# Kernel optimization log

Measured on AMD Instinct MI355X. Metric: run time of the kernel, lower is better.

## Reference

```python
import jax, jax.numpy as jnp
import numpy as np

N_NODES = 50000
N_EDGES = 800000
IN_CH, HID_CH, OUT_CH = 128, 128, 64


def gcn_conv(x, edge_index, edge_weight, W, b, n_nodes):
    """PyG GCNConv: h = D^-1/2 (A + I) D^-1/2 (x @ W) + b, with weighted edges."""
    src, dst = edge_index[0], edge_index[1]
    loop = jnp.arange(n_nodes)
    src_l = jnp.concatenate([src, loop])               # [E+N]
    dst_l = jnp.concatenate([dst, loop])               # [E+N]
    w_l = jnp.concatenate([edge_weight, jnp.ones((n_nodes,), x.dtype)])
    deg = jax.ops.segment_sum(w_l, dst_l, num_segments=n_nodes)  # weighted in-degree incl. self-loop
    dinv = jnp.where(deg > 0, jax.lax.rsqrt(deg), 0.0)
    norm = dinv[src_l] * w_l * dinv[dst_l]             # [E+N]
    h = x @ W                                          # [N, out]
    msg = h[src_l] * norm[:, None]                     # [E+N, out] gather + scale
    out = jax.ops.segment_sum(msg, dst_l, num_segments=n_nodes)  # scatter-add
    return out + b


def setup_inputs() -> dict:
    key = jax.random.key(0)
    k = jax.random.split(key, 8)
    x = jax.random.normal(k[0], (N_NODES, IN_CH), dtype=jnp.float32)
    edge_index = jax.random.randint(k[1], (2, N_EDGES), 0, N_NODES, dtype=jnp.int64)
    edge_weight = jax.random.uniform(k[2], (N_EDGES,), dtype=jnp.float32)
    s1 = 1.0 / np.sqrt(IN_CH)
    s2 = 1.0 / np.sqrt(HID_CH)
    W1 = jax.random.uniform(k[3], (IN_CH, HID_CH), jnp.float32, -s1, s1)
    b1 = jnp.zeros((HID_CH,), jnp.float32)
    W2 = jax.random.uniform(k[4], (HID_CH, OUT_CH), jnp.float32, -s2, s2)
    b2 = jnp.zeros((OUT_CH,), jnp.float32)
    return {"x": x, "edge_index": edge_index, "edge_weight": edge_weight,
            "W1": W1, "b1": b1, "W2": W2, "b2": b2}


def reference(x, edge_index, edge_weight, W1, b1, W2, b2):
    n = x.shape[0]
    h = jax.nn.relu(gcn_conv(x, edge_index, edge_weight, W1, b1, n))
    # dropout(p=0.5) is identity in eval mode
    h = gcn_conv(h, edge_index, edge_weight, W2, b2, n)
    return jax.nn.log_softmax(h, axis=1)
```

## Files before the change

kernel.cpp:

```cpp
#include <hip/hip_runtime.h>
#include <math.h>

static constexpr int CH_IN  = 128;
static constexpr int CH_HID = 128;
static constexpr int CH_OUT = 64;
static constexpr int NBLK1  = 256;

typedef __attribute__((ext_vector_type(8))) short bf16x8;
typedef __attribute__((ext_vector_type(4))) float f32x4;


__device__ __forceinline__ unsigned short f2bf(float f) {
    unsigned int u = __float_as_uint(f);
    u = (u + 0x7fffu + ((u >> 16) & 1u)) >> 16;
    return (unsigned short)u;
}
__device__ __forceinline__ unsigned int pack2(float lo, float hi) {
    return (unsigned int)f2bf(lo) | ((unsigned int)f2bf(hi) << 16);
}
__device__ __forceinline__ void unpack2(unsigned int u, float& lo, float& hi) {
    lo = __uint_as_float(u << 16);
    hi = __uint_as_float(u & 0xffff0000u);
}
__device__ __forceinline__ unsigned int relu2(unsigned int u) {
    unsigned int m = 0;
    if (!(u & 0x8000u)) m |= 0xffffu;
    if (!(u & 0x80000000u)) m |= 0xffff0000u;
    return u & m;
}

__device__ __forceinline__ void gacc8(const uint2* __restrict__ hp, int stride, int s,
                                      int ci, float nm, float* acc) {
    uint2 v = hp[(size_t)s * stride + ci];
    int x = (int)v.x, y = (int)v.y;
    acc[0] = fmaf((float)(char)(x      ), nm, acc[0]);
    acc[1] = fmaf((float)(char)(x >>  8), nm, acc[1]);
    acc[2] = fmaf((float)(char)(x >> 16), nm, acc[2]);
    acc[3] = fmaf((float)(x >> 24),       nm, acc[3]);
    acc[4] = fmaf((float)(char)(y      ), nm, acc[4]);
    acc[5] = fmaf((float)(char)(y >>  8), nm, acc[5]);
    acc[6] = fmaf((float)(char)(y >> 16), nm, acc[6]);
    acc[7] = fmaf((float)(y >> 24),       nm, acc[7]);
}

__device__ __forceinline__ void unq8(uint2 v, float sc, float* hn) {
    int x = (int)v.x, y = (int)v.y;
    hn[0] = (float)(char)(x      ) * sc; hn[1] = (float)(char)(x >>  8) * sc;
    hn[2] = (float)(char)(x >> 16) * sc; hn[3] = (float)(x >> 24)       * sc;
    hn[4] = (float)(char)(y      ) * sc; hn[5] = (float)(char)(y >>  8) * sc;
    hn[6] = (float)(char)(y >> 16) * sc; hn[7] = (float)(y >> 24)       * sc;
}

__device__ __forceinline__ int block_incl_scan_256(int v, int lane, int wid) {
    __shared__ int wtot[4];
    int s = v;
    #pragma unroll
    for (int off = 1; off < 64; off <<= 1) {
        int t = __shfl_up(s, off, 64);
        if (lane >= off) s += t;
    }
    if (lane == 63) wtot[wid] = s;
    __syncthreads();
    int woff = 0;
    for (int j = 0; j < wid; ++j) woff += wtot[j];
    return s + woff;
}


__device__ __forceinline__ void gemm128q_body(const float* __restrict__ X,
                                              const unsigned short* __restrict__ Wt,
                                              signed char* __restrict__ Hq,
                                              float* __restrict__ scl, int N, int blk) {
    constexpr int NCT = CH_HID / 16;
    __shared__ unsigned short As[64 * 136];
    const int tid = threadIdx.x;
    const int lane = tid & 63, wv = tid >> 6;
    const int row0 = blk * 64;

    #pragma unroll
    for (int j = 0; j < 8; ++j) {
        int f = j * 256 + tid;
        int row = f >> 5, col = (f & 31) * 4;
        float4 v = make_float4(0.f, 0.f, 0.f, 0.f);
        if (row0 + row < N)
            v = *reinterpret_cast<const float4*>(X + (size_t)(row0 + row) * CH_IN + col);
        uint2 p;
        p.x = pack2(v.x, v.y);
        p.y = pack2(v.z, v.w);
        *reinterpret_cast<uint2*>(&As[row * 136 + col]) = p;
    }
    __syncthreads();

    const int rw0  = wv * 16;
    const int arow = rw0 + (lane & 15);
    const int kgrp = (lane >> 4) * 8;
    f32x4 acc[NCT];
    #pragma unroll
    for (int c = 0; c < NCT; ++c) acc[c] = f32x4{0.f, 0.f, 0.f, 0.f};

    #pragma unroll
    for (int kk = 0; kk < 4; ++kk) {
        bf16x8 af = *reinterpret_cast<const bf16x8*>(&As[arow * 136 + kk * 32 + kgrp]);
        #pragma unroll
        for (int ct = 0; ct < NCT; ++ct) {
            bf16x8 bf = *reinterpret_cast<const bf16x8*>(
                Wt + (size_t)(ct * 16 + (lane & 15)) * 128 + kk * 32 + kgrp);
            acc[ct] = __builtin_amdgcn_mfma_f32_16x16x32_bf16(af, bf, acc[ct], 0, 0, 0);
        }
    }

    const int orow0 = row0 + rw0 + (lane >> 4) * 4;
    const int ocol  = lane & 15;
    #pragma unroll
    for (int r = 0; r < 4; ++r) {
        float m = 0.f;
        #pragma unroll
        for (int ct = 0; ct < NCT; ++ct) m = fmaxf(m, fabsf(acc[ct][r]));
        m = fmaxf(m, __shfl_xor(m, 1, 64));
        m = fmaxf(m, __shfl_xor(m, 2, 64));
        m = fmaxf(m, __shfl_xor(m, 4, 64));
        m = fmaxf(m, __shfl_xor(m, 8, 64));
        int row = orow0 + r;
        float inv = (m > 0.f) ? 127.f / m : 0.f;
        if (row < N) {
            if (ocol == 0) scl[row] = (m > 0.f) ? m / 127.f : 0.f;
            #pragma unroll
            for (int ct = 0; ct < NCT; ++ct)
                Hq[(size_t)row * CH_HID + ct * 16 + ocol] =
                    (signed char)__float2int_rn(acc[ct][r] * inv);
        }
    }
}


__global__ void k_count(const int* __restrict__ ei, int* __restrict__ cnt_bk,
                        int E, int nbk, int epb,
                        const float* __restrict__ W1, unsigned short* __restrict__ w1t,
                        const float* __restrict__ W2, unsigned short* __restrict__ w2t) {
    __shared__ int bcnt[256];
    const int tid = threadIdx.x;
    if ((int)blockIdx.x < NBLK1) {
        const int b = blockIdx.x;
        bcnt[tid] = 0;
        __syncthreads();
        const int e0 = b * epb, e1 = min(E, e0 + epb);
        for (int e = e0 + tid; e < e1; e += 256)
            atomicAdd(&bcnt[ei[E + e] >> 8], 1);
        __syncthreads();
        if (tid < nbk) cnt_bk[tid * NBLK1 + b] = bcnt[tid];
    } else {
        int j = (blockIdx.x - NBLK1) * 256 + tid;
        if (j < CH_HID * 128) {
            int c = j >> 7, k = j & 127;
            w1t[(size_t)c * 128 + k] = f2bf(W1[(size_t)k * CH_HID + c]);
            return;
        }
        j -= CH_HID * 128;
        if (j < CH_OUT * 128) {
            int c = j >> 7, k = j & 127;
            w2t[(size_t)c * 128 + k] = f2bf(W2[(size_t)k * CH_OUT + c]);
        }
    }
}


__global__ void k_bscan(const int* __restrict__ cnt_bk, int* __restrict__ off_bk,
                        int* __restrict__ btot) {
    const int k = blockIdx.x, tid = threadIdx.x, lane = tid & 63, wid = tid >> 6;
    int c = cnt_bk[k * NBLK1 + tid];
    int incl = block_incl_scan_256(c, lane, wid);
    off_bk[k * NBLK1 + tid] = incl - c;
    if (tid == 255) btot[k] = incl;
}


__global__ void __launch_bounds__(256) k_fat(
        const float* __restrict__ x, const unsigned short* __restrict__ w1t,
        signed char* __restrict__ h1q, float* __restrict__ scl1, int N, int nbg,
        const int* __restrict__ ei, const float* __restrict__ w,
        const int* __restrict__ btot, const int* __restrict__ off_bk,
        uint2* __restrict__ ebuck, int E, int nbk, int epb) {
    if ((int)blockIdx.x < nbg) {
        gemm128q_body(x, w1t, h1q, scl1, N, blockIdx.x);
    } else {
        __shared__ int lcur[256];
        const int b = blockIdx.x - nbg;
        const int tid = threadIdx.x, lane = tid & 63, wid = tid >> 6;
        int v = (tid < nbk) ? btot[tid] : 0;
        int incl = block_incl_scan_256(v, lane, wid);
        if (tid < nbk) lcur[tid] = (incl - v) + off_bk[tid * NBLK1 + b];
        __syncthreads();
        const int e0 = b * epb, e1 = min(E, e0 + epb);
        for (int e = e0 + tid; e < e1; e += 256) {
            unsigned int s = (unsigned int)ei[e];
            unsigned int d = (unsigned int)ei[E + e];
            int pos = atomicAdd(&lcur[d >> 8], 1);
            ebuck[pos] = make_uint2((d << 16) | s, __float_as_uint(w[e]));
        }
    }
}


__global__ void __launch_bounds__(256) k_gemm2(const unsigned short* __restrict__ X,
        const unsigned short* __restrict__ Wt, const float* __restrict__ dinv,
        signed char* __restrict__ Hq, float* __restrict__ ds2, int N) {
    constexpr int COLS = CH_OUT, NCT = COLS / 16;
    __shared__ unsigned short As[64 * 136];
    const int tid = threadIdx.x;
    const int lane = tid & 63, wv = tid >> 6;
    const int row0 = blockIdx.x * 64;

    #pragma unroll
    for (int j = 0; j < 4; ++j) {
        int f = j * 256 + tid;
        int row = f >> 4, col = (f & 15) * 8;
        uint4 v = make_uint4(0u, 0u, 0u, 0u);
        if (row0 + row < N) {
            v = *reinterpret_cast<const uint4*>(X + (size_t)(row0 + row) * CH_IN + col);
            v.x = relu2(v.x); v.y = relu2(v.y);
            v.z = relu2(v.z); v.w = relu2(v.w);
        }
        *reinterpret_cast<uint4*>(&As[row * 136 + col]) = v;
    }
    __syncthreads();

    const int rw0  = wv * 16;
    const int arow = rw0 + (lane & 15);
    const int kgrp = (lane >> 4) * 8;
    f32x4 acc[NCT];
    #pragma unroll
    for (int c = 0; c < NCT; ++c) acc[c] = f32x4{0.f, 0.f, 0.f, 0.f};

    #pragma unroll
    for (int kk = 0; kk < 4; ++kk) {
        bf16x8 af = *reinterpret_cast<const bf16x8*>(&As[arow * 136 + kk * 32 + kgrp]);
        #pragma unroll
        for (int ct = 0; ct < NCT; ++ct) {
            bf16x8 bf = *reinterpret_cast<const bf16x8*>(
                Wt + (size_t)(ct * 16 + (lane & 15)) * 128 + kk * 32 + kgrp);
            acc[ct] = __builtin_amdgcn_mfma_f32_16x16x32_bf16(af, bf, acc[ct], 0, 0, 0);
        }
    }

    const int orow0 = row0 + rw0 + (lane >> 4) * 4;
    const int ocol  = lane & 15;
    #pragma unroll
    for (int r = 0; r < 4; ++r) {
        float m = 0.f;
        #pragma unroll
        for (int ct = 0; ct < NCT; ++ct) m = fmaxf(m, fabsf(acc[ct][r]));
        m = fmaxf(m, __shfl_xor(m, 1, 64));
        m = fmaxf(m, __shfl_xor(m, 2, 64));
        m = fmaxf(m, __shfl_xor(m, 4, 64));
        m = fmaxf(m, __shfl_xor(m, 8, 64));
        int row = orow0 + r;
        float inv = (m > 0.f) ? 127.f / m : 0.f;
        if (row < N) {
            if (ocol == 0) ds2[row] = ((m > 0.f) ? m / 127.f : 0.f) * dinv[row];
            #pragma unroll
            for (int ct = 0; ct < NCT; ++ct)
                Hq[(size_t)row * COLS + ct * 16 + ocol] =
                    (signed char)__float2int_rn(acc[ct][r] * inv);
        }
    }
}


__global__ void k_csr(const uint2* __restrict__ ebuck, const int* __restrict__ btot,
                      const float* __restrict__ scl1, int* __restrict__ rowptr,
                      float* __restrict__ dinv, float* __restrict__ ds1,
                      int2* __restrict__ epack, int N, int nbk) {
    __shared__ int ncnt[256];
    __shared__ float wsm[256];
    __shared__ int ebeg_s, eend_s;
    const int k = blockIdx.x, tid = threadIdx.x, lane = tid & 63, wid = tid >> 6;
    int v = (tid < nbk) ? btot[tid] : 0;
    int incl0 = block_incl_scan_256(v, lane, wid);
    if (tid == k) { ebeg_s = incl0 - v; eend_s = incl0; }
    ncnt[tid] = 0; wsm[tid] = 0.f;
    __syncthreads();
    const int ebeg = ebeg_s, eend = eend_s;
    for (int i = ebeg + tid; i < eend; i += 256) {
        uint2 p = ebuck[i];
        int dl = (p.x >> 16) & 255;
        atomicAdd(&ncnt[dl], 1);
        atomicAdd(&wsm[dl], __uint_as_float(p.y));
    }
    __syncthreads();
    int c = ncnt[tid];
    int incl = block_incl_scan_256(c, lane, wid);
    const int nd = k * 256 + tid;
    if (nd < N) {
        rowptr[nd + 1] = ebeg + incl;
        float dv = rsqrtf(1.0f + wsm[tid]);
        dinv[nd] = dv;
        ds1[nd] = dv * scl1[nd];
    }
    if (k == 0 && tid == 0) rowptr[0] = 0;
    __syncthreads();
    ncnt[tid] = ebeg + incl - c;
    __syncthreads();
    for (int i = ebeg + tid; i < eend; i += 256) {
        uint2 p = ebuck[i];
        int dl = (p.x >> 16) & 255;
        int pos = atomicAdd(&ncnt[dl], 1);
        epack[pos] = make_int2((int)(p.x & 0xFFFFu), (int)p.y);
    }
}


__global__ void k_agg128(const int* __restrict__ rowptr, const int2* __restrict__ epack,
                         const float* __restrict__ dinv, const float* __restrict__ ds1,
                         const signed char* __restrict__ hq,
                         const float* __restrict__ b, unsigned short* __restrict__ out, int N) {
    const int node = (blockIdx.x * blockDim.x + threadIdx.x) >> 6;
    const int lane = threadIdx.x & 63;
    if (node >= N) return;
    const int beg = rowptr[node], end = rowptr[node + 1];
    const float dd = dinv[node];
    const int g  = lane >> 4;
    const int ci = lane & 15;
    const uint2* hp = (const uint2*)hq;

    float acc[8];
    #pragma unroll
    for (int q = 0; q < 8; ++q) acc[q] = 0.f;

    for (int i0 = beg; i0 < end; i0 += 64) {
        const int m = min(64, end - i0);
        int s_l = 0; float nm_l = 0.f;
        if (lane < m) {
            int2 p = epack[i0 + lane];
            s_l = p.x;
            nm_l = __int_as_float(p.y) * ds1[p.x];
        }
        int j = 0;
        for (; j + 16 <= m; j += 16) {
            #pragma unroll
            for (int kk = 0; kk < 4; ++kk) {
                int idx = j + 4 * kk + g;
                int   s  = __shfl(s_l, idx, 64);
                float nm = __shfl(nm_l, idx, 64);
                gacc8(hp, 16, s, ci, nm, acc);
            }
        }
        for (; j < m; j += 4) {
            int idx = j + g;
            int   s  = __shfl(s_l, idx, 64);
            float nm = __shfl(nm_l, idx, 64);
            gacc8(hp, 16, s, ci, nm, acc);
        }
    }
    #pragma unroll
    for (int q = 0; q < 8; ++q) {
        acc[q] += __shfl_xor(acc[q], 16, 64);
        acc[q] += __shfl_xor(acc[q], 32, 64);
    }
    float hn[8];
    unq8(hp[(size_t)node * 16 + ci], ds1[node], hn);
    float4 b0 = *reinterpret_cast<const float4*>(b + 8 * ci);
    float4 b1v = *reinterpret_cast<const float4*>(b + 8 * ci + 4);
    const float bb[8] = {b0.x, b0.y, b0.z, b0.w, b1v.x, b1v.y, b1v.z, b1v.w};
    float res[8];
    #pragma unroll
    for (int q = 0; q < 8; ++q)
        res[q] = fmaf(acc[q] + hn[q], dd, bb[q]);
    if (g == 0) {
        uint4 o;
        o.x = pack2(res[0], res[1]); o.y = pack2(res[2], res[3]);
        o.z = pack2(res[4], res[5]); o.w = pack2(res[6], res[7]);
        ((uint4*)out)[(size_t)node * 16 + ci] = o;
    }
}


__global__ void k_agg64(const int* __restrict__ rowptr, const int2* __restrict__ epack,
                        const float* __restrict__ dinv, const float* __restrict__ ds2,
                        const signed char* __restrict__ hq,
                        const float* __restrict__ b, float* __restrict__ out, int N) {
    const int node = (blockIdx.x * blockDim.x + threadIdx.x) >> 6;
    const int lane = threadIdx.x & 63;
    if (node >= N) return;
    const int beg = rowptr[node], end = rowptr[node + 1];
    const float dd = dinv[node];
    const int g  = lane >> 3;
    const int ci = lane & 7;
    const uint2* hp = (const uint2*)hq;

    float acc[8];
    #pragma unroll
    for (int q = 0; q < 8; ++q) acc[q] = 0.f;

    for (int i0 = beg; i0 < end; i0 += 64) {
        const int m = min(64, end - i0);
        int s_l = 0; float nm_l = 0.f;
        if (lane < m) {
            int2 p = epack[i0 + lane];
            s_l = p.x;
            nm_l = __int_as_float(p.y) * ds2[p.x];
        }
        int j = 0;
        for (; j + 32 <= m; j += 32) {
            #pragma unroll
            for (int kk = 0; kk < 4; ++kk) {
                int idx = j + 8 * kk + g;
                int   s  = __shfl(s_l, idx, 64);
                float nm = __shfl(nm_l, idx, 64);
                gacc8(hp, 8, s, ci, nm, acc);
            }
        }
        for (; j < m; j += 8) {
            int idx = j + g;
            int   s  = __shfl(s_l, idx, 64);
            float nm = __shfl(nm_l, idx, 64);
            gacc8(hp, 8, s, ci, nm, acc);
        }
    }
    #pragma unroll
    for (int q = 0; q < 8; ++q) {
        acc[q] += __shfl_xor(acc[q], 8, 64);
        acc[q] += __shfl_xor(acc[q], 16, 64);
        acc[q] += __shfl_xor(acc[q], 32, 64);
    }
    float hn[8];
    unq8(hp[(size_t)node * 8 + ci], ds2[node], hn);
    float4 b0 = *reinterpret_cast<const float4*>(b + 8 * ci);
    float4 b1v = *reinterpret_cast<const float4*>(b + 8 * ci + 4);
    const float bb[8] = {b0.x, b0.y, b0.z, b0.w, b1v.x, b1v.y, b1v.z, b1v.w};
    float res[8];
    #pragma unroll
    for (int q = 0; q < 8; ++q)
        res[q] = fmaf(acc[q] + hn[q], dd, bb[q]);

    float mx = res[0];
    #pragma unroll
    for (int q = 1; q < 8; ++q) mx = fmaxf(mx, res[q]);
    mx = fmaxf(mx, __shfl_xor(mx, 1, 64));
    mx = fmaxf(mx, __shfl_xor(mx, 2, 64));
    mx = fmaxf(mx, __shfl_xor(mx, 4, 64));
    float sm = 0.f;
    #pragma unroll
    for (int q = 0; q < 8; ++q) sm += expf(res[q] - mx);
    sm += __shfl_xor(sm, 1, 64);
    sm += __shfl_xor(sm, 2, 64);
    sm += __shfl_xor(sm, 4, 64);
    float lse = mx + logf(sm);
    if (g == 0) {
        float4 o0 = make_float4(res[0] - lse, res[1] - lse, res[2] - lse, res[3] - lse);
        float4 o1 = make_float4(res[4] - lse, res[5] - lse, res[6] - lse, res[7] - lse);
        *reinterpret_cast<float4*>(out + (size_t)node * 64 + 8 * ci)     = o0;
        *reinterpret_cast<float4*>(out + (size_t)node * 64 + 8 * ci + 4) = o1;
    }
}

extern "C" void kernel_launch(void* const* d_in, const int* in_sizes, int n_in,
                              void* d_out, int out_size, void* d_ws, size_t ws_size,
                              hipStream_t stream) {
    const float* x  = (const float*)d_in[0];
    const int*   ei = (const int*)d_in[1];
    const float* w  = (const float*)d_in[2];
    const float* W1 = (const float*)d_in[3];
    const float* b1 = (const float*)d_in[4];
    const float* W2 = (const float*)d_in[5];
    const float* b2 = (const float*)d_in[6];
    float* out = (float*)d_out;

    const int N = in_sizes[0] / CH_IN;
    const int E = in_sizes[2];
    const int NBK = (N + 255) >> 8;
    const int EPB = (E + NBLK1 - 1) / NBLK1;
    const int WTB = (CH_HID * 128 + CH_OUT * 128 + 255) / 256;

    float* ws0   = (float*)d_ws;
    float* ws    = ws0;
    float* dinv  = ws;               ws += N;
    float* scl1  = ws;               ws += N;
    float* ds1   = ws;               ws += N;
    float* ds2   = ws;               ws += N;
    int*   rowptr= (int*)ws;         ws += (N + 2);
    int*   cnt_bk= (int*)ws;         ws += 256 * NBLK1;
    int*   off_bk= (int*)ws;         ws += 256 * NBLK1;
    int*   btot  = (int*)ws;         ws += 256;
    uint2* ebuck = (uint2*)ws;       ws += (size_t)2 * E;
    int2*  epack = (int2*)ws;        ws += (size_t)2 * E;
    { size_t off = (size_t)(ws - ws0) & 3; if (off) ws += 4 - off; }
    unsigned short* w1t  = (unsigned short*)ws;  ws += (size_t)CH_HID * 128 / 2;
    unsigned short* w2t  = (unsigned short*)ws;  ws += (size_t)CH_OUT * 128 / 2;
    signed char*    h1q  = (signed char*)ws;     ws += (size_t)N * CH_HID / 4;
    unsigned short* out1 = (unsigned short*)ws;  ws += (size_t)N * CH_HID / 2;
    signed char*    h2q  = (signed char*)ws;     ws += (size_t)N * CH_OUT / 4;

    const int B = 256;

    k_count<<<NBLK1 + WTB, B, 0, stream>>>(ei, cnt_bk, E, NBK, EPB, W1, w1t, W2, w2t);

    k_bscan<<<NBK, 256, 0, stream>>>(cnt_bk, off_bk, btot);

    {
        const int nbg = (N + 63) / 64;
        k_fat<<<nbg + NBLK1, B, 0, stream>>>(x, w1t, h1q, scl1, N, nbg,
                                             ei, w, btot, off_bk, ebuck, E, NBK, EPB);
    }

    k_csr<<<NBK, 256, 0, stream>>>(ebuck, btot, scl1, rowptr, dinv, ds1, epack, N, NBK);

    k_agg128<<<(N * 64 + B - 1) / B, B, 0, stream>>>(rowptr, epack, dinv, ds1, h1q, b1, out1, N);

    k_gemm2<<<(N + 63) / 64, 256, 0, stream>>>(out1, w2t, dinv, h2q, ds2, N);

    k_agg64<<<(N * 64 + B - 1) / B, B, 0, stream>>>(rowptr, epack, dinv, ds2, h2q, b2, out, N);
}
```

Measured before the change: 125.9 us.

## Fuse graph CSR build stages into one cooperative kernel with grid syncs

Merges the edge counting, bucket scan, bucket scatter and per-bucket CSR construction into a single cooperative-launch kernel that uses grid-wide syncs instead of four separate launches. The first-layer GEMM becomes a standalone kernel running after the build, so it can fold dinv into its scale output directly. This cuts kernel launch gaps. In exchange it gives up the previous overlap of GEMM1 with the edge scatter, and the grid is limited to 256 co-resident blocks.

```diff
diff --git a/kernel.cpp b/kernel.cpp
--- a/kernel.cpp
+++ b/kernel.cpp
@@ -1,5 +1,8 @@
 #include <hip/hip_runtime.h>
+#include <hip/hip_cooperative_groups.h>
 #include <math.h>
+
+namespace cg = cooperative_groups;
 
 static constexpr int CH_IN  = 128;
 static constexpr int CH_HID = 128;
@@ -17,10 +20,6 @@
 }
 __device__ __forceinline__ unsigned int pack2(float lo, float hi) {
     return (unsigned int)f2bf(lo) | ((unsigned int)f2bf(hi) << 16);
-}
-__device__ __forceinline__ void unpack2(unsigned int u, float& lo, float& hi) {
-    lo = __uint_as_float(u << 16);
-    hi = __uint_as_float(u & 0xffff0000u);
 }
 __device__ __forceinline__ unsigned int relu2(unsigned int u) {
     unsigned int m = 0;
@@ -67,15 +66,106 @@
 }
 
 
-__device__ __forceinline__ void gemm128q_body(const float* __restrict__ X,
-                                              const unsigned short* __restrict__ Wt,
-                                              signed char* __restrict__ Hq,
-                                              float* __restrict__ scl, int N, int blk) {
+__global__ void __launch_bounds__(256) k_build(
+        const int* __restrict__ ei, const float* __restrict__ w, int E, int nbk, int epb,
+        const float* __restrict__ W1, unsigned short* __restrict__ w1t,
+        const float* __restrict__ W2, unsigned short* __restrict__ w2t,
+        int* __restrict__ cnt_bk, int* __restrict__ off_bk, int* __restrict__ btot,
+        uint2* __restrict__ ebuck, int2* __restrict__ epack,
+        int* __restrict__ rowptr, float* __restrict__ dinv, int N) {
+    cg::grid_group grid = cg::this_grid();
+    __shared__ int sh[256];
+    __shared__ float shf[256];
+    __shared__ int ebeg_s, eend_s;
+    const int b = blockIdx.x, tid = threadIdx.x;
+    const int lane = tid & 63, wid = tid >> 6;
+
+    {
+        int i = b * 256 + tid;
+        if (i < CH_HID * 128) {
+            int c = i >> 7, k = i & 127;
+            w1t[(size_t)c * 128 + k] = f2bf(W1[(size_t)k * CH_HID + c]);
+        } else if (i < CH_HID * 128 + CH_OUT * 128) {
+            int j = i - CH_HID * 128;
+            int c = j >> 7, k = j & 127;
+            w2t[(size_t)c * 128 + k] = f2bf(W2[(size_t)k * CH_OUT + c]);
+        }
+        sh[tid] = 0;
+        __syncthreads();
+        const int e0 = b * epb, e1 = min(E, e0 + epb);
+        for (int e = e0 + tid; e < e1; e += 256)
+            atomicAdd(&sh[ei[E + e] >> 8], 1);
+        __syncthreads();
+        if (tid < nbk) cnt_bk[tid * NBLK1 + b] = sh[tid];
+    }
+    grid.sync();
+
+    if (b < nbk) {
+        int c = cnt_bk[b * NBLK1 + tid];
+        int incl = block_incl_scan_256(c, lane, wid);
+        off_bk[b * NBLK1 + tid] = incl - c;
+        if (tid == 255) btot[b] = incl;
+    }
+    grid.sync();
+
+    {
+        int v = (tid < nbk) ? btot[tid] : 0;
+        int incl = block_incl_scan_256(v, lane, wid);
+        if (tid < nbk) sh[tid] = (incl - v) + off_bk[tid * NBLK1 + b];
+        __syncthreads();
+        const int e0 = b * epb, e1 = min(E, e0 + epb);
+        for (int e = e0 + tid; e < e1; e += 256) {
+            unsigned int s = (unsigned int)ei[e];
+            unsigned int d = (unsigned int)ei[E + e];
+            int pos = atomicAdd(&sh[d >> 8], 1);
+            ebuck[pos] = make_uint2((d << 16) | s, __float_as_uint(w[e]));
+        }
+    }
+    grid.sync();
+
+    if (b < nbk) {
+        int v = (tid < nbk) ? btot[tid] : 0;
+        int incl0 = block_incl_scan_256(v, lane, wid);
+        if (tid == b) { ebeg_s = incl0 - v; eend_s = incl0; }
+        sh[tid] = 0; shf[tid] = 0.f;
+        __syncthreads();
+        const int ebeg = ebeg_s, eend = eend_s;
+        for (int i = ebeg + tid; i < eend; i += 256) {
+            uint2 p = ebuck[i];
+            int dl = (p.x >> 16) & 255;
+            atomicAdd(&sh[dl], 1);
+            atomicAdd(&shf[dl], __uint_as_float(p.y));
+        }
+        __syncthreads();
+        int c = sh[tid];
+        int incl = block_incl_scan_256(c, lane, wid);
+        const int nd = b * 256 + tid;
+        if (nd < N) {
+            rowptr[nd + 1] = ebeg + incl;
+            dinv[nd] = rsqrtf(1.0f + shf[tid]);
+        }
+        if (b == 0 && tid == 0) rowptr[0] = 0;
+        __syncthreads();
+        sh[tid] = ebeg + incl - c;
+        __syncthreads();
+        for (int i = ebeg + tid; i < eend; i += 256) {
+            uint2 p = ebuck[i];
+            int dl = (p.x >> 16) & 255;
+            int pos = atomicAdd(&sh[dl], 1);
+            epack[pos] = make_int2((int)(p.x & 0xFFFFu), (int)p.y);
+        }
+    }
+}
+
+
+__global__ void __launch_bounds__(256) k_gemm1(const float* __restrict__ X,
+        const unsigned short* __restrict__ Wt, const float* __restrict__ dinv,
+        signed char* __restrict__ Hq, float* __restrict__ ds1, int N) {
     constexpr int NCT = CH_HID / 16;
     __shared__ unsigned short As[64 * 136];
     const int tid = threadIdx.x;
     const int lane = tid & 63, wv = tid >> 6;
-    const int row0 = blk * 64;
+    const int row0 = blockIdx.x * 64;
 
     #pragma unroll
     for (int j = 0; j < 8; ++j) {
@@ -123,79 +213,11 @@
         int row = orow0 + r;
         float inv = (m > 0.f) ? 127.f / m : 0.f;
         if (row < N) {
-            if (ocol == 0) scl[row] = (m > 0.f) ? m / 127.f : 0.f;
+            if (ocol == 0) ds1[row] = ((m > 0.f) ? m / 127.f : 0.f) * dinv[row];
             #pragma unroll
             for (int ct = 0; ct < NCT; ++ct)
                 Hq[(size_t)row * CH_HID + ct * 16 + ocol] =
                     (signed char)__float2int_rn(acc[ct][r] * inv);
-        }
-    }
-}
-
-
-__global__ void k_count(const int* __restrict__ ei, int* __restrict__ cnt_bk,
-                        int E, int nbk, int epb,
-                        const float* __restrict__ W1, unsigned short* __restrict__ w1t,
-                        const float* __restrict__ W2, unsigned short* __restrict__ w2t) {
-    __shared__ int bcnt[256];
-    const int tid = threadIdx.x;
-    if ((int)blockIdx.x < NBLK1) {
-        const int b = blockIdx.x;
-        bcnt[tid] = 0;
-        __syncthreads();
-        const int e0 = b * epb, e1 = min(E, e0 + epb);
-        for (int e = e0 + tid; e < e1; e += 256)
-            atomicAdd(&bcnt[ei[E + e] >> 8], 1);
-        __syncthreads();
-        if (tid < nbk) cnt_bk[tid * NBLK1 + b] = bcnt[tid];
-    } else {
-        int j = (blockIdx.x - NBLK1) * 256 + tid;
-        if (j < CH_HID * 128) {
-            int c = j >> 7, k = j & 127;
-            w1t[(size_t)c * 128 + k] = f2bf(W1[(size_t)k * CH_HID + c]);
-            return;
-        }
-        j -= CH_HID * 128;
-        if (j < CH_OUT * 128) {
-            int c = j >> 7, k = j & 127;
-            w2t[(size_t)c * 128 + k] = f2bf(W2[(size_t)k * CH_OUT + c]);
-        }
-    }
-}
-
-
-__global__ void k_bscan(const int* __restrict__ cnt_bk, int* __restrict__ off_bk,
-                        int* __restrict__ btot) {
-    const int k = blockIdx.x, tid = threadIdx.x, lane = tid & 63, wid = tid >> 6;
-    int c = cnt_bk[k * NBLK1 + tid];
-    int incl = block_incl_scan_256(c, lane, wid);
-    off_bk[k * NBLK1 + tid] = incl - c;
-    if (tid == 255) btot[k] = incl;
-}
-
-
-__global__ void __launch_bounds__(256) k_fat(
-        const float* __restrict__ x, const unsigned short* __restrict__ w1t,
-        signed char* __restrict__ h1q, float* __restrict__ scl1, int N, int nbg,
-        const int* __restrict__ ei, const float* __restrict__ w,
-        const int* __restrict__ btot, const int* __restrict__ off_bk,
-        uint2* __restrict__ ebuck, int E, int nbk, int epb) {
-    if ((int)blockIdx.x < nbg) {
-        gemm128q_body(x, w1t, h1q, scl1, N, blockIdx.x);
-    } else {
-        __shared__ int lcur[256];
-        const int b = blockIdx.x - nbg;
-        const int tid = threadIdx.x, lane = tid & 63, wid = tid >> 6;
-        int v = (tid < nbk) ? btot[tid] : 0;
-        int incl = block_incl_scan_256(v, lane, wid);
-        if (tid < nbk) lcur[tid] = (incl - v) + off_bk[tid * NBLK1 + b];
-        __syncthreads();
-        const int e0 = b * epb, e1 = min(E, e0 + epb);
-        for (int e = e0 + tid; e < e1; e += 256) {
-            unsigned int s = (unsigned int)ei[e];
-            unsigned int d = (unsigned int)ei[E + e];
-            int pos = atomicAdd(&lcur[d >> 8], 1);
-            ebuck[pos] = make_uint2((d << 16) | s, __float_as_uint(w[e]));
         }
     }
 }
@@ -266,49 +288,6 @@
 }
 
 
-__global__ void k_csr(const uint2* __restrict__ ebuck, const int* __restrict__ btot,
-                      const float* __restrict__ scl1, int* __restrict__ rowptr,
-                      float* __restrict__ dinv, float* __restrict__ ds1,
-                      int2* __restrict__ epack, int N, int nbk) {
-    __shared__ int ncnt[256];
-    __shared__ float wsm[256];
-    __shared__ int ebeg_s, eend_s;
-    const int k = blockIdx.x, tid = threadIdx.x, lane = tid & 63, wid = tid >> 6;
-    int v = (tid < nbk) ? btot[tid] : 0;
-    int incl0 = block_incl_scan_256(v, lane, wid);
-    if (tid == k) { ebeg_s = incl0 - v; eend_s = incl0; }
-    ncnt[tid] = 0; wsm[tid] = 0.f;
-    __syncthreads();
-    const int ebeg = ebeg_s, eend = eend_s;
-    for (int i = ebeg + tid; i < eend; i += 256) {
-        uint2 p = ebuck[i];
-        int dl = (p.x >> 16) & 255;
-        atomicAdd(&ncnt[dl], 1);
-        atomicAdd(&wsm[dl], __uint_as_float(p.y));
-    }
-    __syncthreads();
-    int c = ncnt[tid];
-    int incl = block_incl_scan_256(c, lane, wid);
-    const int nd = k * 256 + tid;
-    if (nd < N) {
-        rowptr[nd + 1] = ebeg + incl;
-        float dv = rsqrtf(1.0f + wsm[tid]);
-        dinv[nd] = dv;
-        ds1[nd] = dv * scl1[nd];
-    }
-    if (k == 0 && tid == 0) rowptr[0] = 0;
-    __syncthreads();
-    ncnt[tid] = ebeg + incl - c;
-    __syncthreads();
-    for (int i = ebeg + tid; i < eend; i += 256) {
-        uint2 p = ebuck[i];
-        int dl = (p.x >> 16) & 255;
-        int pos = atomicAdd(&ncnt[dl], 1);
-        epack[pos] = make_int2((int)(p.x & 0xFFFFu), (int)p.y);
-    }
-}
-
-
 __global__ void k_agg128(const int* __restrict__ rowptr, const int2* __restrict__ epack,
                          const float* __restrict__ dinv, const float* __restrict__ ds1,
                          const signed char* __restrict__ hq,
@@ -469,12 +448,10 @@
     const int E = in_sizes[2];
     const int NBK = (N + 255) >> 8;
     const int EPB = (E + NBLK1 - 1) / NBLK1;
-    const int WTB = (CH_HID * 128 + CH_OUT * 128 + 255) / 256;
 
     float* ws0   = (float*)d_ws;
     float* ws    = ws0;
     float* dinv  = ws;               ws += N;
-    float* scl1  = ws;               ws += N;
     float* ds1   = ws;               ws += N;
     float* ds2   = ws;               ws += N;
     int*   rowptr= (int*)ws;         ws += (N + 2);
@@ -492,21 +469,22 @@
 
     const int B = 256;
 
-    k_count<<<NBLK1 + WTB, B, 0, stream>>>(ei, cnt_bk, E, NBK, EPB, W1, w1t, W2, w2t);
-
-    k_bscan<<<NBK, 256, 0, stream>>>(cnt_bk, off_bk, btot);
-
     {
-        const int nbg = (N + 63) / 64;
-        k_fat<<<nbg + NBLK1, B, 0, stream>>>(x, w1t, h1q, scl1, N, nbg,
-                                             ei, w, btot, off_bk, ebuck, E, NBK, EPB);
-    }
-
-    k_csr<<<NBK, 256, 0, stream>>>(ebuck, btot, scl1, rowptr, dinv, ds1, epack, N, NBK);
+        int E_v = E, nbk_v = NBK, epb_v = EPB, N_v = N;
+        void* args[] = {
+            (void*)&ei, (void*)&w, (void*)&E_v, (void*)&nbk_v, (void*)&epb_v,
+            (void*)&W1, (void*)&w1t, (void*)&W2, (void*)&w2t,
+            (void*)&cnt_bk, (void*)&off_bk, (void*)&btot,
+            (void*)&ebuck, (void*)&epack, (void*)&rowptr, (void*)&dinv, (void*)&N_v
+        };
+        hipLaunchCooperativeKernel((void*)k_build, dim3(NBLK1), dim3(B), args, 0, stream);
+    }
+
+    k_gemm1<<<(N + 63) / 64, B, 0, stream>>>(x, w1t, dinv, h1q, ds1, N);
 
     k_agg128<<<(N * 64 + B - 1) / B, B, 0, stream>>>(rowptr, epack, dinv, ds1, h1q, b1, out1, N);
 
-    k_gemm2<<<(N + 63) / 64, 256, 0, stream>>>(out1, w2t, dinv, h2q, ds2, N);
+    k_gemm2<<<(N + 63) / 64, B, 0, stream>>>(out1, w2t, dinv, h2q, ds2, N);
 
     k_agg64<<<(N * 64 + B - 1) / B, B, 0, stream>>>(rowptr, epack, dinv, ds2, h2q, b2, out, N);
 }
```

Result: slower. 238.6 us (+89.5%).
